# Optimization experiments

Hardware: AMD Instinct MI355X
Metric: run time of the kernel (lower is better)

The kernel has to match this reference:

```python
import jax, jax.numpy as jnp
import numpy as np

D_MODEL = 2048
D_HEAD = 128
NUM_HEADS = 16
D_KV_LATENT = 512
BATCH = 2
SEQ = 2048


def setup_inputs() -> dict:
    key = jax.random.key(0)
    ks = jax.random.split(key, 6)
    s = 0.02
    return {
        "x": jax.random.normal(ks[0], (BATCH, SEQ, D_MODEL), jnp.float32),
        "Wd": jax.random.normal(ks[1], (D_KV_LATENT, D_MODEL), jnp.float32) * s,
        "Wuk": jax.random.normal(ks[2], (NUM_HEADS * D_HEAD, D_KV_LATENT), jnp.float32) * s,
        "Wuv": jax.random.normal(ks[3], (NUM_HEADS * D_HEAD, D_KV_LATENT), jnp.float32) * s,
        "Wq": jax.random.normal(ks[4], (NUM_HEADS * D_HEAD, D_MODEL), jnp.float32) * s,
        "Wo": jax.random.normal(ks[5], (D_MODEL, NUM_HEADS * D_HEAD), jnp.float32) * s,
        "use_cache": 1,
    }


def _mla_cache_path(x, Wd, Wuk, Wuv, Wq, Wo):
    # Weight-absorbed MLA prefill from an empty cache (total_seq_len == seq_len).
    b, s, dm = x.shape
    h, dh, c = NUM_HEADS, D_HEAD, D_KV_LATENT
    # latents = downsample(x): [b, s, c]
    latents = jnp.einsum("bsm,cm->bsc", x, Wd)
    # absorbed weights: q_uk [h, dm, c], out_uv [h, dm, c]
    q_uk = jnp.einsum("hdm,hdc->hmc", Wq.reshape(h, dh, dm), Wuk.reshape(h, dh, c))
    out_uv = jnp.einsum("mhd,hdc->hmc", Wo.reshape(dm, h, dh), Wuv.reshape(h, dh, c))
    # query_part: [b, h, s, c]
    query_part = jnp.einsum("bsm,hmc->bhsc", x, q_uk)
    # value_part: [b, h, s, dm]
    value_part = jnp.einsum("hmc,btc->bhtm", out_uv, latents)
    # scores over latent dim: [b, h, s, s]
    scores = jnp.einsum("bhsc,btc->bhst", query_part, latents) / np.sqrt(dh).astype(np.float32)
    causal = jnp.triu(jnp.ones((s, s), dtype=bool), k=1)
    scores = jnp.where(causal, -jnp.inf, scores)
    attn = jax.nn.softmax(scores, axis=-1)
    # output already in model dim; sum contributions over heads
    out = jnp.einsum("bhst,bhtm->bsm", attn, value_part)
    return out


def reference(x, Wd, Wuk, Wuv, Wq, Wo, use_cache):
    # use_cache is a static Python int (1 -> weight-absorbed cache path)
    return _mla_cache_path(x, Wd, Wuk, Wuv, Wq, Wo)
```

## Files before the change

### kernel.cpp

```cpp
#include <hip/hip_runtime.h>
#include <hip/hip_bf16.h>

typedef __attribute__((ext_vector_type(8))) short short8x;
typedef __attribute__((ext_vector_type(4))) float f32x4;

__device__ __forceinline__ ushort f2bf(float f){
  union { __hip_bfloat16 b; ushort u; } cvt;
  cvt.b = __float2bfloat16(f);
  return cvt.u;
}

__global__ __launch_bounds__(256) void cvt_kernel(const float* __restrict__ in, ushort* __restrict__ out, long n){
  long i = ((long)blockIdx.x * 256 + threadIdx.x) * 4;
  if (i >= n) return;
  float4 v = *(const float4*)(in + i);
  ushort4 o;
  o.x = f2bf(v.x); o.y = f2bf(v.y); o.z = f2bf(v.z); o.w = f2bf(v.w);
  *(ushort4*)(out + i) = o;
}

template<int OUTBF>
__global__ __launch_bounds__(256, 3)
void gemm_bt(const ushort* __restrict__ A, const ushort* __restrict__ BT, void* __restrict__ Cv,
             int M, int N, int K, int lda, int ldb, int ldc,
             long aZ, long bZ, long cZ, float scale)
{
  __shared__ __align__(16) ushort As[2][128 * 32];
  __shared__ __align__(16) ushort Bs[2][128 * 32];
  const int z = blockIdx.z;
  const ushort* Ab = A + (long)z * aZ;
  const ushort* Bb = BT + (long)z * bZ;
  const int tid = threadIdx.x, lane = tid & 63, w = tid >> 6;
  const int wm = w >> 1, wn = w & 1;
  const int lq = lane & 15, q4 = lane >> 4;

  int lin = blockIdx.x + gridDim.x * blockIdx.y;
  const int cpx = (gridDim.x * gridDim.y) >> 3;
  lin = (lin & 7) * cpx + (lin >> 3);
  const int bx = lin % gridDim.x, by = lin / gridDim.x;

  const long arow = (long)by * 128, brow = (long)bx * 128;
  const int lr = lane >> 2, lc = (lane & 3) * 8;

  const f32x4 z4 = {0.f, 0.f, 0.f, 0.f};
  f32x4 acc[4][4];
#pragma unroll
  for (int i = 0; i < 4; i++)
#pragma unroll
    for (int j = 0; j < 4; j++) acc[i][j] = z4;

  auto stage = [&](int buf, int k0){
#pragma unroll
    for (int is = 0; is < 2; ++is){
      const int rb = is * 64 + w * 16;
      const ushort* ga = Ab + (arow + rb + lr) * (long)lda + k0 + lc;
      const ushort* gb = Bb + (brow + rb + lr) * (long)ldb + k0 + lc;
      __builtin_amdgcn_global_load_lds((const __attribute__((address_space(1))) void*)ga,
                                       (__attribute__((address_space(3))) void*)&As[buf][rb * 32], 16, 0, 0);
      __builtin_amdgcn_global_load_lds((const __attribute__((address_space(1))) void*)gb,
                                       (__attribute__((address_space(3))) void*)&Bs[buf][rb * 32], 16, 0, 0);
    }
  };

  const int nk = K >> 5;
  stage(0, 0);
  for (int kt = 0; kt < nk; ++kt){
    __syncthreads();
    if (kt + 1 < nk) stage((kt + 1) & 1, (kt + 1) * 32);
    const int buf = kt & 1;
    short8x a[4], b[4];
#pragma unroll
    for (int i = 0; i < 4; i++){
      a[i] = *(const short8x*)&As[buf][(wm * 64 + i * 16 + lq) * 32 + q4 * 8];
      b[i] = *(const short8x*)&Bs[buf][(wn * 64 + i * 16 + lq) * 32 + q4 * 8];
    }
#pragma unroll
    for (int i = 0; i < 4; i++)
#pragma unroll
      for (int j = 0; j < 4; j++)
        acc[i][j] = __builtin_amdgcn_mfma_f32_16x16x32_bf16(a[i], b[j], acc[i][j], 0, 0, 0);
  }

  const long crowb = arow + wm * 64;
  const long ccolb = brow + wn * 64;
#pragma unroll
  for (int i = 0; i < 4; i++)
#pragma unroll
    for (int j = 0; j < 4; j++)
#pragma unroll
      for (int r = 0; r < 4; r++){
        const long row = crowb + i * 16 + q4 * 4 + r;
        const long col = ccolb + j * 16 + lq;
        const float v = acc[i][j][r] * scale;
        if (OUTBF) ((ushort*)Cv)[(long)z * cZ + row * ldc + col] = f2bf(v);
        else       ((float*)Cv)[(long)z * cZ + row * ldc + col] = v;
      }
}

__global__ __launch_bounds__(512, 2)
void flash7_kernel(const ushort* __restrict__ q, const ushort* __restrict__ k,
                   const ushort* __restrict__ vT, ushort* __restrict__ attnO)
{
  __shared__ __align__(16) ushort Kb[2][64 * 128];
  __shared__ __align__(16) ushort Vb[2][128 * 64];
  __shared__ __align__(16) ushort Pl[8][2][16][72];

  const int tid = threadIdx.x, lane = tid & 63, w = tid >> 6;
  const int lq = lane & 15, q4 = lane >> 4;

  const int xcd = blockIdx.x & 7;
  const int bh = xcd * 4 + ((blockIdx.x >> 3) & 3);
  const int qb = blockIdx.x >> 5;
  const int b = bh & 1, h = bh >> 1;

  const int nt = (qb + 1) * 4;
  const int wd = qb * 4 + (w >> 1);
  const int moff = (w & 1) * 32;

  const ushort* kb_ = k + (long)b * 2048 * 2048 + h * 128;
  const ushort* vb_ = vT + (long)h * 128 * 4096 + (long)b * 2048;

  const ushort* kbase[2]; const ushort* vbase[2]; int kofs[2], vofs[2];
#pragma unroll
  for (int is = 0; is < 2; ++is){
    const int ofse = is * 4096 + w * 512;
    const int krow = (ofse >> 7) + (lane >> 4);
    const int kg = (lane & 15) ^ (krow & 7);
    kbase[is] = kb_ + (long)krow * 2048 + kg * 8;
    kofs[is] = ofse;
    const int drow = (ofse >> 6) + (lane >> 3);
    const int vg = (lane & 7) ^ (drow & 7);
    vbase[is] = vb_ + (long)drow * 4096 + vg * 8;
    vofs[is] = ofse;
  }

  auto stage = [&](int buf, int tt){
    const long t0 = (long)tt * 64;
#pragma unroll
    for (int is = 0; is < 2; ++is){
      __builtin_amdgcn_global_load_lds((const __attribute__((address_space(1))) void*)(kbase[is] + t0 * 2048),
          (__attribute__((address_space(3))) void*)&Kb[buf][kofs[is]], 16, 0, 0);
      __builtin_amdgcn_global_load_lds((const __attribute__((address_space(1))) void*)(vbase[is] + t0),
          (__attribute__((address_space(3))) void*)&Vb[buf][vofs[is]], 16, 0, 0);
    }
  };

  const f32x4 z4 = {0.f, 0.f, 0.f, 0.f};

  const int qrow0 = qb * 256 + w * 32;
  const long qgbase = (long)b * 2048 + qrow0;

  short8x qf[2][4];
#pragma unroll
  for (int si = 0; si < 2; si++){
    const ushort* qp = q + (qgbase + si * 16 + lq) * 2048 + h * 128 + q4 * 8;
#pragma unroll
    for (int ks = 0; ks < 4; ks++) qf[si][ks] = *(const short8x*)(qp + ks * 32);
  }

  f32x4 oacc[8][2];
#pragma unroll
  for (int dt = 0; dt < 8; dt++){ oacc[dt][0] = z4; oacc[dt][1] = z4; }
  float dsum0 = 0.f, dsum1 = 0.f;

  stage(0, 0);
  stage(1, 1);

#pragma unroll 1
  for (int tt = 0; tt < nt; ++tt){
    if (tt == nt - 1) asm volatile("s_waitcnt vmcnt(0)" ::: "memory");
    else              asm volatile("s_waitcnt vmcnt(4)" ::: "memory");
    __syncthreads();
    const int cur = tt & 1;

    if (tt <= wd){
      short8x ak[4][4];
#pragma unroll
      for (int ti = 0; ti < 4; ti++){
        const int r = ti * 16 + lq;
        const int rb = r * 128;
        const int rx = r & 7;
#pragma unroll
        for (int ks = 0; ks < 4; ks++)
          ak[ti][ks] = *(const short8x*)&Kb[cur][rb + (((ks * 4 + q4) ^ rx) * 8)];
      }
      f32x4 st[4][2];
#pragma unroll
      for (int ti = 0; ti < 4; ti++){ st[ti][0] = z4; st[ti][1] = z4; }
#pragma unroll
      for (int ks = 0; ks < 4; ks++)
#pragma unroll
        for (int ti = 0; ti < 4; ti++)
#pragma unroll
          for (int si = 0; si < 2; si++)
            st[ti][si] = __builtin_amdgcn_mfma_f32_16x16x32_bf16(ak[ti][ks], qf[si][ks], st[ti][si], 0, 0, 0);

      const bool diag = (tt == wd);
#pragma unroll
      for (int si = 0; si < 2; si++){
#pragma unroll
        for (int ti = 0; ti < 4; ti++){
          ushort4 pb;
#pragma unroll
          for (int r = 0; r < 4; r++){
            const int tl = ti * 16 + q4 * 4 + r;
            float p = __expf(st[ti][si][r]);
            if (diag && tl > moff + si * 16 + lq) p = 0.f;
            if (si) dsum1 += p; else dsum0 += p;
            ((ushort*)&pb)[r] = f2bf(p);
          }
          *(ushort4*)&Pl[w][si][lq][ti * 16 + q4 * 4] = pb;
        }
        asm volatile("s_waitcnt lgkmcnt(0)" ::: "memory");
        __builtin_amdgcn_sched_barrier(0);
        const short8x pf0 = *(const short8x*)&Pl[w][si][lq][q4 * 8];
        const short8x pf1 = *(const short8x*)&Pl[w][si][lq][32 + q4 * 8];
        __builtin_amdgcn_sched_barrier(0);
#pragma unroll
        for (int dt = 0; dt < 8; dt++){
          const int r = dt * 16 + lq;
          const int rb = r * 64;
          const int rx = lq & 7;
          const short8x av0 = *(const short8x*)&Vb[cur][rb + (((0 * 4 + q4) ^ rx) * 8)];
          const short8x av1 = *(const short8x*)&Vb[cur][rb + (((1 * 4 + q4) ^ rx) * 8)];
          oacc[dt][si] = __builtin_amdgcn_mfma_f32_16x16x32_bf16(av0, pf0, oacc[dt][si], 0, 0, 0);
          oacc[dt][si] = __builtin_amdgcn_mfma_f32_16x16x32_bf16(av1, pf1, oacc[dt][si], 0, 0, 0);
        }
      }
    }
    __syncthreads();
    if (tt + 2 < nt) stage(cur, tt + 2);
  }

  dsum0 += __shfl_xor(dsum0, 16); dsum0 += __shfl_xor(dsum0, 32);
  dsum1 += __shfl_xor(dsum1, 16); dsum1 += __shfl_xor(dsum1, 32);
  const float inv0 = 1.f / dsum0, inv1 = 1.f / dsum1;

#pragma unroll
  for (int dt = 0; dt < 8; dt++)
#pragma unroll
    for (int si = 0; si < 2; si++){
      const float inv = si ? inv1 : inv0;
      ushort4 o;
      o.x = f2bf(oacc[dt][si][0] * inv);
      o.y = f2bf(oacc[dt][si][1] * inv);
      o.z = f2bf(oacc[dt][si][2] * inv);
      o.w = f2bf(oacc[dt][si][3] * inv);
      *(ushort4*)(attnO + (qgbase + si * 16 + lq) * 2048 + h * 128 + dt * 16 + q4 * 4) = o;
    }
}

extern "C" void kernel_launch(void* const* d_in, const int* in_sizes, int n_in,
                              void* d_out, int out_size, void* d_ws, size_t ws_size,
                              hipStream_t stream)
{
  const float* x   = (const float*)d_in[0];
  const float* Wd  = (const float*)d_in[1];
  const float* Wuk = (const float*)d_in[2];
  const float* Wuv = (const float*)d_in[3];
  const float* Wq  = (const float*)d_in[4];
  const float* Wo  = (const float*)d_in[5];
  float* out = (float*)d_out;
  ushort* ws = (ushort*)d_ws;

  ushort* xb    = ws + 0L;
  ushort* wdb   = ws + 8388608L;
  ushort* wqb   = ws + 9437184L;
  ushort* wob   = ws + 13631488L;
  ushort* wukb  = ws + 17825792L;
  ushort* wuvb  = ws + 18874368L;
  ushort* lat   = ws + 19922944L;
  ushort* qb    = ws + 22020096L;
  ushort* kb    = ws + 30408704L;
  ushort* vTb   = ws + 38797312L;
  ushort* attnO = ws + 47185920L;

  cvt_kernel<<<8192, 256, 0, stream>>>(x,   xb,   8388608L);
  cvt_kernel<<<1024, 256, 0, stream>>>(Wd,  wdb,  1048576L);
  cvt_kernel<<<4096, 256, 0, stream>>>(Wq,  wqb,  4194304L);
  cvt_kernel<<<4096, 256, 0, stream>>>(Wo,  wob,  4194304L);
  cvt_kernel<<<1024, 256, 0, stream>>>(Wuk, wukb, 1048576L);
  cvt_kernel<<<1024, 256, 0, stream>>>(Wuv, wuvb, 1048576L);

  gemm_bt<1><<<dim3(4, 32, 1), 256, 0, stream>>>(xb, wdb, lat, 4096, 512, 2048,
      2048, 2048, 512, 0L, 0L, 0L, 1.0f);
  gemm_bt<1><<<dim3(16, 32, 1), 256, 0, stream>>>(xb, wqb, qb, 4096, 2048, 2048,
      2048, 2048, 2048, 0L, 0L, 0L, 0.08838834764831845f);
  gemm_bt<1><<<dim3(16, 32, 1), 256, 0, stream>>>(lat, wukb, kb, 4096, 2048, 512,
      512, 512, 2048, 0L, 0L, 0L, 1.0f);
  gemm_bt<1><<<dim3(32, 16, 1), 256, 0, stream>>>(wuvb, lat, vTb, 2048, 4096, 512,
      512, 512, 4096, 0L, 0L, 0L, 1.0f);
  flash7_kernel<<<256, 512, 0, stream>>>(qb, kb, vTb, attnO);
  gemm_bt<0><<<dim3(16, 32, 1), 256, 0, stream>>>(attnO, wob, out, 4096, 2048, 2048,
      2048, 2048, 2048, 0L, 0L, 0L, 1.0f);
}
```

Baseline: 278.2 us.

## Fuse Q and latent projections, software-pipeline QK with PV in flash kernel

Concatenates Wq (pre-scaled by softmax scale times log2e) and Wd into one weight matrix so a single GEMM produces both Q and latents into a strided buffer. The flash kernel now uses exp2f and software-pipelines the loop: the QK MFMA for tile t runs alongside the softmax and PV of tile t-1, with raised wave priority. The V buffer grows to four slots so the lagged PV step reads valid data. This costs more LDS and registers and adds epilogue handling for the last diagonal tile.

```diff
diff --git a/kernel.cpp b/kernel.cpp
--- a/kernel.cpp
+++ b/kernel.cpp
@@ -10,12 +10,13 @@
   return cvt.u;
 }
 
-__global__ __launch_bounds__(256) void cvt_kernel(const float* __restrict__ in, ushort* __restrict__ out, long n){
+__global__ __launch_bounds__(256) void cvt_kernel(const float* __restrict__ in, ushort* __restrict__ out,
+                                                  long n, float scale){
   long i = ((long)blockIdx.x * 256 + threadIdx.x) * 4;
   if (i >= n) return;
   float4 v = *(const float4*)(in + i);
   ushort4 o;
-  o.x = f2bf(v.x); o.y = f2bf(v.y); o.z = f2bf(v.z); o.w = f2bf(v.w);
+  o.x = f2bf(v.x * scale); o.y = f2bf(v.y * scale); o.z = f2bf(v.z * scale); o.w = f2bf(v.w * scale);
   *(ushort4*)(out + i) = o;
 }
 
@@ -98,11 +99,11 @@
 }
 
 __global__ __launch_bounds__(512, 2)
-void flash7_kernel(const ushort* __restrict__ q, const ushort* __restrict__ k,
+void flash8_kernel(const ushort* __restrict__ q, const ushort* __restrict__ k,
                    const ushort* __restrict__ vT, ushort* __restrict__ attnO)
 {
   __shared__ __align__(16) ushort Kb[2][64 * 128];
-  __shared__ __align__(16) ushort Vb[2][128 * 64];
+  __shared__ __align__(16) ushort Vb[4][128 * 64];
   __shared__ __align__(16) ushort Pl[8][2][16][72];
 
   const int tid = threadIdx.x, lane = tid & 63, w = tid >> 6;
@@ -134,14 +135,14 @@
     vofs[is] = ofse;
   }
 
-  auto stage = [&](int buf, int tt){
+  auto stage = [&](int kbuf, int vbuf, int tt){
     const long t0 = (long)tt * 64;
 #pragma unroll
     for (int is = 0; is < 2; ++is){
       __builtin_amdgcn_global_load_lds((const __attribute__((address_space(1))) void*)(kbase[is] + t0 * 2048),
-          (__attribute__((address_space(3))) void*)&Kb[buf][kofs[is]], 16, 0, 0);
+          (__attribute__((address_space(3))) void*)&Kb[kbuf][kofs[is]], 16, 0, 0);
       __builtin_amdgcn_global_load_lds((const __attribute__((address_space(1))) void*)(vbase[is] + t0),
-          (__attribute__((address_space(3))) void*)&Vb[buf][vofs[is]], 16, 0, 0);
+          (__attribute__((address_space(3))) void*)&Vb[vbuf][vofs[is]], 16, 0, 0);
     }
   };
 
@@ -153,7 +154,7 @@
   short8x qf[2][4];
 #pragma unroll
   for (int si = 0; si < 2; si++){
-    const ushort* qp = q + (qgbase + si * 16 + lq) * 2048 + h * 128 + q4 * 8;
+    const ushort* qp = q + (qgbase + si * 16 + lq) * 2560 + h * 128 + q4 * 8;
 #pragma unroll
     for (int ks = 0; ks < 4; ks++) qf[si][ks] = *(const short8x*)(qp + ks * 32);
   }
@@ -162,74 +163,110 @@
 #pragma unroll
   for (int dt = 0; dt < 8; dt++){ oacc[dt][0] = z4; oacc[dt][1] = z4; }
   float dsum0 = 0.f, dsum1 = 0.f;
-
-  stage(0, 0);
-  stage(1, 1);
+  f32x4 stA[4][2], stB[4][2];
+
+  auto qk_load = [&](int cur, short8x (&ak)[4][4]){
+#pragma unroll
+    for (int ti = 0; ti < 4; ti++){
+      const int r = ti * 16 + lq;
+      const int rb = r * 128;
+      const int rx = r & 7;
+#pragma unroll
+      for (int ks = 0; ks < 4; ks++)
+        ak[ti][ks] = *(const short8x*)&Kb[cur][rb + (((ks * 4 + q4) ^ rx) * 8)];
+    }
+  };
+  auto qk_mfma = [&](short8x (&ak)[4][4], f32x4 (&st)[4][2]){
+#pragma unroll
+    for (int ti = 0; ti < 4; ti++){ st[ti][0] = z4; st[ti][1] = z4; }
+#pragma unroll
+    for (int ks = 0; ks < 4; ks++)
+#pragma unroll
+      for (int ti = 0; ti < 4; ti++)
+#pragma unroll
+        for (int si = 0; si < 2; si++)
+          st[ti][si] = __builtin_amdgcn_mfma_f32_16x16x32_bf16(ak[ti][ks], qf[si][ks], st[ti][si], 0, 0, 0);
+  };
+  auto fin_pack = [&](f32x4 (&st)[4][2], bool diag){
+#pragma unroll
+    for (int si = 0; si < 2; si++)
+#pragma unroll
+      for (int ti = 0; ti < 4; ti++){
+        ushort4 pb;
+#pragma unroll
+        for (int r = 0; r < 4; r++){
+          const int tl = ti * 16 + q4 * 4 + r;
+          float p = exp2f(st[ti][si][r]);
+          if (diag && tl > moff + si * 16 + lq) p = 0.f;
+          if (si) dsum1 += p; else dsum0 += p;
+          ((ushort*)&pb)[r] = f2bf(p);
+        }
+        *(ushort4*)&Pl[w][si][lq][ti * 16 + q4 * 4] = pb;
+      }
+  };
+  auto fin_pv = [&](int vbuf){
+#pragma unroll
+    for (int si = 0; si < 2; si++){
+      const short8x pf0 = *(const short8x*)&Pl[w][si][lq][q4 * 8];
+      const short8x pf1 = *(const short8x*)&Pl[w][si][lq][32 + q4 * 8];
+#pragma unroll
+      for (int dt = 0; dt < 8; dt++){
+        const int r = dt * 16 + lq;
+        const int rb = r * 64;
+        const int rx = lq & 7;
+        const short8x av0 = *(const short8x*)&Vb[vbuf][rb + (((q4) ^ rx) * 8)];
+        const short8x av1 = *(const short8x*)&Vb[vbuf][rb + (((4 + q4) ^ rx) * 8)];
+        oacc[dt][si] = __builtin_amdgcn_mfma_f32_16x16x32_bf16(av0, pf0, oacc[dt][si], 0, 0, 0);
+        oacc[dt][si] = __builtin_amdgcn_mfma_f32_16x16x32_bf16(av1, pf1, oacc[dt][si], 0, 0, 0);
+      }
+    }
+  };
+
+  stage(0, 0, 0);
+  stage(1, 1, 1);
 
 #pragma unroll 1
   for (int tt = 0; tt < nt; ++tt){
     if (tt == nt - 1) asm volatile("s_waitcnt vmcnt(0)" ::: "memory");
     else              asm volatile("s_waitcnt vmcnt(4)" ::: "memory");
     __syncthreads();
-    const int cur = tt & 1;
 
     if (tt <= wd){
       short8x ak[4][4];
-#pragma unroll
-      for (int ti = 0; ti < 4; ti++){
-        const int r = ti * 16 + lq;
-        const int rb = r * 128;
-        const int rx = r & 7;
-#pragma unroll
-        for (int ks = 0; ks < 4; ks++)
-          ak[ti][ks] = *(const short8x*)&Kb[cur][rb + (((ks * 4 + q4) ^ rx) * 8)];
-      }
-      f32x4 st[4][2];
-#pragma unroll
-      for (int ti = 0; ti < 4; ti++){ st[ti][0] = z4; st[ti][1] = z4; }
-#pragma unroll
-      for (int ks = 0; ks < 4; ks++)
-#pragma unroll
-        for (int ti = 0; ti < 4; ti++)
-#pragma unroll
-          for (int si = 0; si < 2; si++)
-            st[ti][si] = __builtin_amdgcn_mfma_f32_16x16x32_bf16(ak[ti][ks], qf[si][ks], st[ti][si], 0, 0, 0);
-
-      const bool diag = (tt == wd);
-#pragma unroll
-      for (int si = 0; si < 2; si++){
-#pragma unroll
-        for (int ti = 0; ti < 4; ti++){
-          ushort4 pb;
-#pragma unroll
-          for (int r = 0; r < 4; r++){
-            const int tl = ti * 16 + q4 * 4 + r;
-            float p = __expf(st[ti][si][r]);
-            if (diag && tl > moff + si * 16 + lq) p = 0.f;
-            if (si) dsum1 += p; else dsum0 += p;
-            ((ushort*)&pb)[r] = f2bf(p);
-          }
-          *(ushort4*)&Pl[w][si][lq][ti * 16 + q4 * 4] = pb;
-        }
+      qk_load(tt & 1, ak);
+      if (tt == 0){
+        qk_mfma(ak, stA);
+      } else if (tt & 1){
+        fin_pack(stA, false);
         asm volatile("s_waitcnt lgkmcnt(0)" ::: "memory");
         __builtin_amdgcn_sched_barrier(0);
-        const short8x pf0 = *(const short8x*)&Pl[w][si][lq][q4 * 8];
-        const short8x pf1 = *(const short8x*)&Pl[w][si][lq][32 + q4 * 8];
+        __builtin_amdgcn_s_setprio(1);
+        qk_mfma(ak, stB);
+        fin_pv((tt - 1) & 3);
+        __builtin_amdgcn_s_setprio(0);
+      } else {
+        fin_pack(stB, false);
+        asm volatile("s_waitcnt lgkmcnt(0)" ::: "memory");
         __builtin_amdgcn_sched_barrier(0);
-#pragma unroll
-        for (int dt = 0; dt < 8; dt++){
-          const int r = dt * 16 + lq;
-          const int rb = r * 64;
-          const int rx = lq & 7;
-          const short8x av0 = *(const short8x*)&Vb[cur][rb + (((0 * 4 + q4) ^ rx) * 8)];
-          const short8x av1 = *(const short8x*)&Vb[cur][rb + (((1 * 4 + q4) ^ rx) * 8)];
-          oacc[dt][si] = __builtin_amdgcn_mfma_f32_16x16x32_bf16(av0, pf0, oacc[dt][si], 0, 0, 0);
-          oacc[dt][si] = __builtin_amdgcn_mfma_f32_16x16x32_bf16(av1, pf1, oacc[dt][si], 0, 0, 0);
-        }
+        __builtin_amdgcn_s_setprio(1);
+        qk_mfma(ak, stA);
+        fin_pv((tt - 1) & 3);
+        __builtin_amdgcn_s_setprio(0);
       }
+    } else if (tt == wd + 1){
+      if (wd & 1) fin_pack(stB, true); else fin_pack(stA, true);
+      asm volatile("s_waitcnt lgkmcnt(0)" ::: "memory");
+      __builtin_amdgcn_sched_barrier(0);
+      fin_pv(wd & 3);
     }
     __syncthreads();
-    if (tt + 2 < nt) stage(cur, tt + 2);
+    if (tt + 2 < nt) stage(tt & 1, (tt + 2) & 3, tt + 2);
+  }
+  if (wd == nt - 1){
+    fin_pack(stB, true);
+    asm volatile("s_waitcnt lgkmcnt(0)" ::: "memory");
+    __builtin_amdgcn_sched_barrier(0);
+    fin_pv(wd & 3);
   }
 
   dsum0 += __shfl_xor(dsum0, 16); dsum0 += __shfl_xor(dsum0, 32);
@@ -264,33 +301,31 @@
   ushort* ws = (ushort*)d_ws;
 
   ushort* xb    = ws + 0L;
-  ushort* wdb   = ws + 8388608L;
-  ushort* wqb   = ws + 9437184L;
+  ushort* wqdb  = ws + 8388608L;
   ushort* wob   = ws + 13631488L;
   ushort* wukb  = ws + 17825792L;
   ushort* wuvb  = ws + 18874368L;
-  ushort* lat   = ws + 19922944L;
-  ushort* qb    = ws + 22020096L;
+  ushort* qlat  = ws + 19922944L;
   ushort* kb    = ws + 30408704L;
   ushort* vTb   = ws + 38797312L;
   ushort* attnO = ws + 47185920L;
 
-  cvt_kernel<<<8192, 256, 0, stream>>>(x,   xb,   8388608L);
-  cvt_kernel<<<1024, 256, 0, stream>>>(Wd,  wdb,  1048576L);
-  cvt_kernel<<<4096, 256, 0, stream>>>(Wq,  wqb,  4194304L);
-  cvt_kernel<<<4096, 256, 0, stream>>>(Wo,  wob,  4194304L);
-  cvt_kernel<<<1024, 256, 0, stream>>>(Wuk, wukb, 1048576L);
-  cvt_kernel<<<1024, 256, 0, stream>>>(Wuv, wuvb, 1048576L);
-
-  gemm_bt<1><<<dim3(4, 32, 1), 256, 0, stream>>>(xb, wdb, lat, 4096, 512, 2048,
-      2048, 2048, 512, 0L, 0L, 0L, 1.0f);
-  gemm_bt<1><<<dim3(16, 32, 1), 256, 0, stream>>>(xb, wqb, qb, 4096, 2048, 2048,
-      2048, 2048, 2048, 0L, 0L, 0L, 0.08838834764831845f);
-  gemm_bt<1><<<dim3(16, 32, 1), 256, 0, stream>>>(lat, wukb, kb, 4096, 2048, 512,
-      512, 512, 2048, 0L, 0L, 0L, 1.0f);
-  gemm_bt<1><<<dim3(32, 16, 1), 256, 0, stream>>>(wuvb, lat, vTb, 2048, 4096, 512,
-      512, 512, 4096, 0L, 0L, 0L, 1.0f);
-  flash7_kernel<<<256, 512, 0, stream>>>(qb, kb, vTb, attnO);
+  const float QSCL = 0.12751744800f;
+
+  cvt_kernel<<<8192, 256, 0, stream>>>(x,   xb,            8388608L, 1.0f);
+  cvt_kernel<<<4096, 256, 0, stream>>>(Wq,  wqdb,          4194304L, QSCL);
+  cvt_kernel<<<1024, 256, 0, stream>>>(Wd,  wqdb + 4194304L, 1048576L, 1.0f);
+  cvt_kernel<<<4096, 256, 0, stream>>>(Wo,  wob,           4194304L, 1.0f);
+  cvt_kernel<<<1024, 256, 0, stream>>>(Wuk, wukb,          1048576L, 1.0f);
+  cvt_kernel<<<1024, 256, 0, stream>>>(Wuv, wuvb,          1048576L, 1.0f);
+
+  gemm_bt<1><<<dim3(20, 32, 1), 256, 0, stream>>>(xb, wqdb, qlat, 4096, 2560, 2048,
+      2048, 2048, 2560, 0L, 0L, 0L, 1.0f);
+  gemm_bt<1><<<dim3(16, 32, 1), 256, 0, stream>>>(qlat + 2048, wukb, kb, 4096, 2048, 512,
+      2560, 512, 2048, 0L, 0L, 0L, 1.0f);
+  gemm_bt<1><<<dim3(32, 16, 1), 256, 0, stream>>>(wuvb, qlat + 2048, vTb, 2048, 4096, 512,
+      512, 2560, 4096, 0L, 0L, 0L, 1.0f);
+  flash8_kernel<<<256, 512, 0, stream>>>(qlat, kb, vTb, attnO);
   gemm_bt<0><<<dim3(16, 32, 1), 256, 0, stream>>>(attnO, wob, out, 4096, 2048, 2048,
       2048, 2048, 2048, 0L, 0L, 0L, 1.0f);
 }
```

Result: slower. 560.1 us (+101.4%).

## Fuse Q and latent projections into one GEMM and widen flash attention waves

Applied to the files above, without the earlier changes.

Concatenates the Wq and Wd weights so a single GEMM produces both the queries and the latents in one interleaved buffer with row stride 2560. The softmax scale times log2(e) is folded into the Wq conversion so the attention kernel can use exp2f. The flash kernel moves from 512 threads with 32 query rows per wave to 256 threads with 64 rows per wave, reusing each K fragment load across four query subtiles. This removes one GEMM launch and a second read of x, and cuts LDS K reads per query. In exchange it raises register pressure and halves the waves per block, which may reduce latency hiding.

```diff
diff --git a/kernel.cpp b/kernel.cpp
--- a/kernel.cpp
+++ b/kernel.cpp
@@ -10,12 +10,13 @@
   return cvt.u;
 }
 
-__global__ __launch_bounds__(256) void cvt_kernel(const float* __restrict__ in, ushort* __restrict__ out, long n){
+__global__ __launch_bounds__(256) void cvt_kernel(const float* __restrict__ in, ushort* __restrict__ out,
+                                                  long n, float scale){
   long i = ((long)blockIdx.x * 256 + threadIdx.x) * 4;
   if (i >= n) return;
   float4 v = *(const float4*)(in + i);
   ushort4 o;
-  o.x = f2bf(v.x); o.y = f2bf(v.y); o.z = f2bf(v.z); o.w = f2bf(v.w);
+  o.x = f2bf(v.x * scale); o.y = f2bf(v.y * scale); o.z = f2bf(v.z * scale); o.w = f2bf(v.w * scale);
   *(ushort4*)(out + i) = o;
 }
 
@@ -97,13 +98,13 @@
       }
 }
 
-__global__ __launch_bounds__(512, 2)
-void flash7_kernel(const ushort* __restrict__ q, const ushort* __restrict__ k,
-                   const ushort* __restrict__ vT, ushort* __restrict__ attnO)
+__global__ __launch_bounds__(256, 1)
+void flash10_kernel(const ushort* __restrict__ q, const ushort* __restrict__ k,
+                    const ushort* __restrict__ vT, ushort* __restrict__ attnO)
 {
   __shared__ __align__(16) ushort Kb[2][64 * 128];
   __shared__ __align__(16) ushort Vb[2][128 * 64];
-  __shared__ __align__(16) ushort Pl[8][2][16][72];
+  __shared__ __align__(16) ushort Pl[4][4][16][72];
 
   const int tid = threadIdx.x, lane = tid & 63, w = tid >> 6;
   const int lq = lane & 15, q4 = lane >> 4;
@@ -114,54 +115,52 @@
   const int b = bh & 1, h = bh >> 1;
 
   const int nt = (qb + 1) * 4;
-  const int wd = qb * 4 + (w >> 1);
-  const int moff = (w & 1) * 32;
+  const int wdiag = qb * 4 + w;
 
   const ushort* kb_ = k + (long)b * 2048 * 2048 + h * 128;
   const ushort* vb_ = vT + (long)h * 128 * 4096 + (long)b * 2048;
 
-  const ushort* kbase[2]; const ushort* vbase[2]; int kofs[2], vofs[2];
-#pragma unroll
-  for (int is = 0; is < 2; ++is){
-    const int ofse = is * 4096 + w * 512;
-    const int krow = (ofse >> 7) + (lane >> 4);
-    const int kg = (lane & 15) ^ (krow & 7);
-    kbase[is] = kb_ + (long)krow * 2048 + kg * 8;
-    kofs[is] = ofse;
-    const int drow = (ofse >> 6) + (lane >> 3);
-    const int vg = (lane & 7) ^ (drow & 7);
-    vbase[is] = vb_ + (long)drow * 4096 + vg * 8;
-    vofs[is] = ofse;
-  }
+  const int krow0 = w * 4 + (lane >> 4);
+  const int kg = (lane & 15) ^ (krow0 & 7);
+  const ushort* kbase = kb_ + (long)krow0 * 2048 + kg * 8;
+  const int kofs0 = w * 512;
+
+  const int drow0 = w * 8 + (lane >> 3);
+  const int vg = (lane & 7) ^ (drow0 & 7);
+  const ushort* vbase = vb_ + (long)drow0 * 4096 + vg * 8;
+  const int vofs0 = w * 512;
 
   auto stage = [&](int buf, int tt){
-    const long t0 = (long)tt * 64;
-#pragma unroll
-    for (int is = 0; is < 2; ++is){
-      __builtin_amdgcn_global_load_lds((const __attribute__((address_space(1))) void*)(kbase[is] + t0 * 2048),
-          (__attribute__((address_space(3))) void*)&Kb[buf][kofs[is]], 16, 0, 0);
-      __builtin_amdgcn_global_load_lds((const __attribute__((address_space(1))) void*)(vbase[is] + t0),
-          (__attribute__((address_space(3))) void*)&Vb[buf][vofs[is]], 16, 0, 0);
+    const ushort* kp = kbase + (long)tt * 64 * 2048;
+    const ushort* vp = vbase + (long)tt * 64;
+#pragma unroll
+    for (int is = 0; is < 4; ++is){
+      __builtin_amdgcn_global_load_lds((const __attribute__((address_space(1))) void*)(kp + (long)is * 16 * 2048),
+          (__attribute__((address_space(3))) void*)&Kb[buf][kofs0 + is * 2048], 16, 0, 0);
+      __builtin_amdgcn_global_load_lds((const __attribute__((address_space(1))) void*)(vp + (long)is * 32 * 4096),
+          (__attribute__((address_space(3))) void*)&Vb[buf][vofs0 + is * 2048], 16, 0, 0);
     }
   };
 
   const f32x4 z4 = {0.f, 0.f, 0.f, 0.f};
 
-  const int qrow0 = qb * 256 + w * 32;
+  const int qrow0 = qb * 256 + w * 64;
   const long qgbase = (long)b * 2048 + qrow0;
 
-  short8x qf[2][4];
-#pragma unroll
-  for (int si = 0; si < 2; si++){
-    const ushort* qp = q + (qgbase + si * 16 + lq) * 2048 + h * 128 + q4 * 8;
+  short8x qf[4][4];
+#pragma unroll
+  for (int si = 0; si < 4; si++){
+    const ushort* qp = q + (qgbase + si * 16 + lq) * 2560 + h * 128 + q4 * 8;
 #pragma unroll
     for (int ks = 0; ks < 4; ks++) qf[si][ks] = *(const short8x*)(qp + ks * 32);
   }
 
-  f32x4 oacc[8][2];
-#pragma unroll
-  for (int dt = 0; dt < 8; dt++){ oacc[dt][0] = z4; oacc[dt][1] = z4; }
-  float dsum0 = 0.f, dsum1 = 0.f;
+  f32x4 oacc[8][4];
+#pragma unroll
+  for (int dt = 0; dt < 8; dt++)
+#pragma unroll
+    for (int si = 0; si < 4; si++) oacc[dt][si] = z4;
+  float dsum[4] = {0.f, 0.f, 0.f, 0.f};
 
   stage(0, 0);
   stage(1, 1);
@@ -169,62 +168,58 @@
 #pragma unroll 1
   for (int tt = 0; tt < nt; ++tt){
     if (tt == nt - 1) asm volatile("s_waitcnt vmcnt(0)" ::: "memory");
-    else              asm volatile("s_waitcnt vmcnt(4)" ::: "memory");
+    else              asm volatile("s_waitcnt vmcnt(8)" ::: "memory");
     __syncthreads();
     const int cur = tt & 1;
 
-    if (tt <= wd){
-      short8x ak[4][4];
-#pragma unroll
-      for (int ti = 0; ti < 4; ti++){
+    if (tt <= wdiag){
+      const bool diag = (tt == wdiag);
+#pragma unroll
+      for (int ti = 0; ti < 4; ++ti){
         const int r = ti * 16 + lq;
         const int rb = r * 128;
         const int rx = r & 7;
-#pragma unroll
-        for (int ks = 0; ks < 4; ks++)
-          ak[ti][ks] = *(const short8x*)&Kb[cur][rb + (((ks * 4 + q4) ^ rx) * 8)];
-      }
-      f32x4 st[4][2];
-#pragma unroll
-      for (int ti = 0; ti < 4; ti++){ st[ti][0] = z4; st[ti][1] = z4; }
-#pragma unroll
-      for (int ks = 0; ks < 4; ks++)
-#pragma unroll
-        for (int ti = 0; ti < 4; ti++)
-#pragma unroll
-          for (int si = 0; si < 2; si++)
-            st[ti][si] = __builtin_amdgcn_mfma_f32_16x16x32_bf16(ak[ti][ks], qf[si][ks], st[ti][si], 0, 0, 0);
-
-      const bool diag = (tt == wd);
-#pragma unroll
-      for (int si = 0; si < 2; si++){
-#pragma unroll
-        for (int ti = 0; ti < 4; ti++){
+        const short8x a0 = *(const short8x*)&Kb[cur][rb + (((q4) ^ rx) * 8)];
+        const short8x a1 = *(const short8x*)&Kb[cur][rb + (((4 + q4) ^ rx) * 8)];
+        const short8x a2 = *(const short8x*)&Kb[cur][rb + (((8 + q4) ^ rx) * 8)];
+        const short8x a3 = *(const short8x*)&Kb[cur][rb + (((12 + q4) ^ rx) * 8)];
+#pragma unroll
+        for (int si = 0; si < 4; ++si){
+          f32x4 st = __builtin_amdgcn_mfma_f32_16x16x32_bf16(a0, qf[si][0], z4, 0, 0, 0);
+          st = __builtin_amdgcn_mfma_f32_16x16x32_bf16(a1, qf[si][1], st, 0, 0, 0);
+          st = __builtin_amdgcn_mfma_f32_16x16x32_bf16(a2, qf[si][2], st, 0, 0, 0);
+          st = __builtin_amdgcn_mfma_f32_16x16x32_bf16(a3, qf[si][3], st, 0, 0, 0);
           ushort4 pb;
 #pragma unroll
-          for (int r = 0; r < 4; r++){
-            const int tl = ti * 16 + q4 * 4 + r;
-            float p = __expf(st[ti][si][r]);
-            if (diag && tl > moff + si * 16 + lq) p = 0.f;
-            if (si) dsum1 += p; else dsum0 += p;
-            ((ushort*)&pb)[r] = f2bf(p);
+          for (int r4 = 0; r4 < 4; ++r4){
+            const int tl = ti * 16 + q4 * 4 + r4;
+            float p = exp2f(st[r4]);
+            if (diag && tl > si * 16 + lq) p = 0.f;
+            dsum[si] += p;
+            ((ushort*)&pb)[r4] = f2bf(p);
           }
           *(ushort4*)&Pl[w][si][lq][ti * 16 + q4 * 4] = pb;
         }
-        asm volatile("s_waitcnt lgkmcnt(0)" ::: "memory");
-        __builtin_amdgcn_sched_barrier(0);
-        const short8x pf0 = *(const short8x*)&Pl[w][si][lq][q4 * 8];
-        const short8x pf1 = *(const short8x*)&Pl[w][si][lq][32 + q4 * 8];
-        __builtin_amdgcn_sched_barrier(0);
-#pragma unroll
-        for (int dt = 0; dt < 8; dt++){
+      }
+      asm volatile("s_waitcnt lgkmcnt(0)" ::: "memory");
+      __builtin_amdgcn_sched_barrier(0);
+#pragma unroll
+      for (int sp = 0; sp < 2; ++sp){
+        const short8x pf00 = *(const short8x*)&Pl[w][2 * sp][lq][q4 * 8];
+        const short8x pf01 = *(const short8x*)&Pl[w][2 * sp][lq][32 + q4 * 8];
+        const short8x pf10 = *(const short8x*)&Pl[w][2 * sp + 1][lq][q4 * 8];
+        const short8x pf11 = *(const short8x*)&Pl[w][2 * sp + 1][lq][32 + q4 * 8];
+#pragma unroll
+        for (int dt = 0; dt < 8; ++dt){
           const int r = dt * 16 + lq;
           const int rb = r * 64;
           const int rx = lq & 7;
-          const short8x av0 = *(const short8x*)&Vb[cur][rb + (((0 * 4 + q4) ^ rx) * 8)];
-          const short8x av1 = *(const short8x*)&Vb[cur][rb + (((1 * 4 + q4) ^ rx) * 8)];
-          oacc[dt][si] = __builtin_amdgcn_mfma_f32_16x16x32_bf16(av0, pf0, oacc[dt][si], 0, 0, 0);
-          oacc[dt][si] = __builtin_amdgcn_mfma_f32_16x16x32_bf16(av1, pf1, oacc[dt][si], 0, 0, 0);
+          const short8x av0 = *(const short8x*)&Vb[cur][rb + (((q4) ^ rx) * 8)];
+          const short8x av1 = *(const short8x*)&Vb[cur][rb + (((4 + q4) ^ rx) * 8)];
+          oacc[dt][2 * sp]     = __builtin_amdgcn_mfma_f32_16x16x32_bf16(av0, pf00, oacc[dt][2 * sp], 0, 0, 0);
+          oacc[dt][2 * sp]     = __builtin_amdgcn_mfma_f32_16x16x32_bf16(av1, pf01, oacc[dt][2 * sp], 0, 0, 0);
+          oacc[dt][2 * sp + 1] = __builtin_amdgcn_mfma_f32_16x16x32_bf16(av0, pf10, oacc[dt][2 * sp + 1], 0, 0, 0);
+          oacc[dt][2 * sp + 1] = __builtin_amdgcn_mfma_f32_16x16x32_bf16(av1, pf11, oacc[dt][2 * sp + 1], 0, 0, 0);
         }
       }
     }
@@ -232,20 +227,24 @@
     if (tt + 2 < nt) stage(cur, tt + 2);
   }
 
-  dsum0 += __shfl_xor(dsum0, 16); dsum0 += __shfl_xor(dsum0, 32);
-  dsum1 += __shfl_xor(dsum1, 16); dsum1 += __shfl_xor(dsum1, 32);
-  const float inv0 = 1.f / dsum0, inv1 = 1.f / dsum1;
+  float inv[4];
+#pragma unroll
+  for (int si = 0; si < 4; ++si){
+    float d = dsum[si];
+    d += __shfl_xor(d, 16);
+    d += __shfl_xor(d, 32);
+    inv[si] = 1.f / d;
+  }
 
 #pragma unroll
   for (int dt = 0; dt < 8; dt++)
 #pragma unroll
-    for (int si = 0; si < 2; si++){
-      const float inv = si ? inv1 : inv0;
+    for (int si = 0; si < 4; si++){
       ushort4 o;
-      o.x = f2bf(oacc[dt][si][0] * inv);
-      o.y = f2bf(oacc[dt][si][1] * inv);
-      o.z = f2bf(oacc[dt][si][2] * inv);
-      o.w = f2bf(oacc[dt][si][3] * inv);
+      o.x = f2bf(oacc[dt][si][0] * inv[si]);
+      o.y = f2bf(oacc[dt][si][1] * inv[si]);
+      o.z = f2bf(oacc[dt][si][2] * inv[si]);
+      o.w = f2bf(oacc[dt][si][3] * inv[si]);
       *(ushort4*)(attnO + (qgbase + si * 16 + lq) * 2048 + h * 128 + dt * 16 + q4 * 4) = o;
     }
 }
@@ -264,33 +263,31 @@
   ushort* ws = (ushort*)d_ws;
 
   ushort* xb    = ws + 0L;
-  ushort* wdb   = ws + 8388608L;
-  ushort* wqb   = ws + 9437184L;
+  ushort* wqdb  = ws + 8388608L;
   ushort* wob   = ws + 13631488L;
   ushort* wukb  = ws + 17825792L;
   ushort* wuvb  = ws + 18874368L;
-  ushort* lat   = ws + 19922944L;
-  ushort* qb    = ws + 22020096L;
+  ushort* qlat  = ws + 19922944L;
   ushort* kb    = ws + 30408704L;
   ushort* vTb   = ws + 38797312L;
   ushort* attnO = ws + 47185920L;
 
-  cvt_kernel<<<8192, 256, 0, stream>>>(x,   xb,   8388608L);
-  cvt_kernel<<<1024, 256, 0, stream>>>(Wd,  wdb,  1048576L);
-  cvt_kernel<<<4096, 256, 0, stream>>>(Wq,  wqb,  4194304L);
-  cvt_kernel<<<4096, 256, 0, stream>>>(Wo,  wob,  4194304L);
-  cvt_kernel<<<1024, 256, 0, stream>>>(Wuk, wukb, 1048576L);
-  cvt_kernel<<<1024, 256, 0, stream>>>(Wuv, wuvb, 1048576L);
-
-  gemm_bt<1><<<dim3(4, 32, 1), 256, 0, stream>>>(xb, wdb, lat, 4096, 512, 2048,
-      2048, 2048, 512, 0L, 0L, 0L, 1.0f);
-  gemm_bt<1><<<dim3(16, 32, 1), 256, 0, stream>>>(xb, wqb, qb, 4096, 2048, 2048,
-      2048, 2048, 2048, 0L, 0L, 0L, 0.08838834764831845f);
-  gemm_bt<1><<<dim3(16, 32, 1), 256, 0, stream>>>(lat, wukb, kb, 4096, 2048, 512,
-      512, 512, 2048, 0L, 0L, 0L, 1.0f);
-  gemm_bt<1><<<dim3(32, 16, 1), 256, 0, stream>>>(wuvb, lat, vTb, 2048, 4096, 512,
-      512, 512, 4096, 0L, 0L, 0L, 1.0f);
-  flash7_kernel<<<256, 512, 0, stream>>>(qb, kb, vTb, attnO);
+  const float QSCL = 0.12751744800f;
+
+  cvt_kernel<<<8192, 256, 0, stream>>>(x,   xb,            8388608L, 1.0f);
+  cvt_kernel<<<4096, 256, 0, stream>>>(Wq,  wqdb,          4194304L, QSCL);
+  cvt_kernel<<<1024, 256, 0, stream>>>(Wd,  wqdb + 4194304L, 1048576L, 1.0f);
+  cvt_kernel<<<4096, 256, 0, stream>>>(Wo,  wob,           4194304L, 1.0f);
+  cvt_kernel<<<1024, 256, 0, stream>>>(Wuk, wukb,          1048576L, 1.0f);
+  cvt_kernel<<<1024, 256, 0, stream>>>(Wuv, wuvb,          1048576L, 1.0f);
+
+  gemm_bt<1><<<dim3(20, 32, 1), 256, 0, stream>>>(xb, wqdb, qlat, 4096, 2560, 2048,
+      2048, 2048, 2560, 0L, 0L, 0L, 1.0f);
+  gemm_bt<1><<<dim3(16, 32, 1), 256, 0, stream>>>(qlat + 2048, wukb, kb, 4096, 2048, 512,
+      2560, 512, 2048, 0L, 0L, 0L, 1.0f);
+  gemm_bt<1><<<dim3(32, 16, 1), 256, 0, stream>>>(wuvb, qlat + 2048, vTb, 2048, 4096, 512,
+      512, 2560, 4096, 0L, 0L, 0L, 1.0f);
+  flash10_kernel<<<256, 256, 0, stream>>>(qlat, kb, vTb, attnO);
   gemm_bt<0><<<dim3(16, 32, 1), 256, 0, stream>>>(attnO, wob, out, 4096, 2048, 2048,
       2048, 2048, 2048, 0L, 0L, 0L, 1.0f);
 }
```

Measured after the change: 271.6 us. 1.02x faster.
